# Optimization experiments

Measured on AMD Instinct MI355X. Metric: run time of the kernel, lower is better.

## Reference

```python
import jax, jax.numpy as jnp
import numpy as np

N = 8192
NT = 85       # number of DFIRE atom types
BINS = 28     # distance bins, d/0.7 clamped to [0,27]
EXCLU = 2     # nbre_nt_exclu


def setup_inputs() -> dict:
    key = jax.random.key(0)
    k1, k2, k3, k4 = jax.random.split(key, 4)
    # coords scaled so pairwise distances span the 0..19.6A cutoff range
    coords = jax.random.normal(k1, (N, 3), dtype=jnp.float32) * 10.0
    res_ids = jnp.sort(jax.random.randint(k2, (N,), 0, 400)).astype(jnp.int32)
    type_indices = jax.random.randint(k3, (N,), 0, NT).astype(jnp.int32)
    pot = jax.random.normal(k4, (NT, NT, BINS), dtype=jnp.float32)
    # original LUT is symmetric in the two type axes
    pot_tensor = 0.5 * (pot + jnp.transpose(pot, (1, 0, 2)))
    # upper-triangular pair indices, offset=1 (deterministic, like torch.triu_indices)
    ii, jj = np.triu_indices(N, 1)
    i_idx = jnp.asarray(ii, dtype=jnp.int32)
    j_idx = jnp.asarray(jj, dtype=jnp.int32)
    return {
        "coords": coords,
        "pot_tensor": pot_tensor,
        "res_ids": res_ids,
        "type_indices": type_indices,
        "i_idx": i_idx,
        "j_idx": j_idx,
    }


def reference(coords, pot_tensor, res_ids, type_indices, i_idx, j_idx):
    # sequence-separation and valid-type mask (stream compaction -> masked sum)
    sep = jnp.abs(res_ids[i_idx] - res_ids[j_idx])
    t1 = type_indices[i_idx]
    t2 = type_indices[j_idx]
    mask = (sep > EXCLU) & (t1 >= 0) & (t2 >= 0)

    # pairwise distances on all triu pairs
    diff = coords[i_idx] - coords[j_idx]              # [P,3]
    dists = jnp.sqrt(jnp.sum(diff * diff, axis=1)) + 1e-8  # [P]

    # bin + linear interpolation from the 3D LUT
    d_scaled = dists / 0.7
    d0 = jnp.floor(jnp.clip(d_scaled, 0.0, 27.0)).astype(jnp.int32)
    d1 = jnp.minimum(d0 + 1, 27)
    alpha = d_scaled - d0.astype(dists.dtype)

    # safe indices for masked-out pairs (their energy is multiplied by 0)
    t1s = jnp.where(mask, t1, 0)
    t2s = jnp.where(mask, t2, 0)
    e0 = pot_tensor[t1s, t2s, d0]
    e1 = pot_tensor[t1s, t2s, d1]
    energy = (1.0 - alpha) * e0 + alpha * e1

    w = mask & (dists < 19.6)
    return jnp.sum(energy * w.astype(energy.dtype))
```

## Files before the change

kernel.cpp:

```cpp
#include <hip/hip_runtime.h>

#define NT    85
#define BINS  28
#define LUT_ELEMS (NT * NT * BINS)
#define CUT2  (19.6f * 19.6f)
#define ROWCAP 8
#define COLCAP 8

__device__ __forceinline__ unsigned bf16r(float x) {
    unsigned b = __float_as_uint(x);
    return (b + 0x7FFFu + ((b >> 16) & 1u)) >> 16;
}

__global__ __launch_bounds__(256) void prep_k(const float* __restrict__ pot,
                                              const int* __restrict__ type, int N,
                                              unsigned* __restrict__ pk,
                                              int* __restrict__ offs) {
    if ((int)blockIdx.x == (int)gridDim.x - 1) {
        __shared__ int h[NT];
        for (int t = threadIdx.x; t < NT; t += 256) h[t] = 0;
        __syncthreads();
        for (int i = threadIdx.x; i < N; i += 256) atomicAdd(&h[type[i]], 1);
        __syncthreads();
        if (threadIdx.x == 0) {
            int s = 0;
            for (int t = 0; t < NT; ++t) { int c = h[t]; offs[t] = s; s += c; }
        }
    }
    int idx = blockIdx.x * 256 + threadIdx.x;
    if (idx < LUT_ELEMS) {
        int d  = idx % BINS;
        int ab = idx / BINS;
        int d1 = (d + 1 < BINS) ? d + 1 : BINS - 1;
        float e0 = pot[idx], e1 = pot[ab * BINS + d1];
        pk[idx] = (bf16r(e1) << 16) | bf16r(e0);
    }
}

__global__ void scatter_k(const float* __restrict__ coords, const int* __restrict__ res,
                          const int* __restrict__ type, int* __restrict__ offs,
                          float4* __restrict__ pc, int N) {
    int i = blockIdx.x * blockDim.x + threadIdx.x;
    if (i >= N) return;
    int t = type[i];
    int p = atomicAdd(&offs[t], 1);
    pc[p] = make_float4(coords[3 * i], coords[3 * i + 1], coords[3 * i + 2],
                        __int_as_float((t << 10) | res[i]));
}

__global__ __launch_bounds__(128) void dfire_pairs6(
    const float4*  __restrict__ pc,
    const unsigned* __restrict__ pk,
    float* __restrict__ partial, int TI, int TJ) {

    __shared__ float4   jtile[128];
    __shared__ unsigned lrow[ROWCAP * COLCAP * BINS];
    __shared__ float    wsum[2];

    int k = blockIdx.x;
    double A = (double)TJ + 1.0;
    int ri = (int)((A - sqrt(A * A - 4.0 * (double)k)) * 0.5);
    if (ri < 0) ri = 0;
    if (ri > TI - 1) ri = TI - 1;
    while (ri > 0 && ri * (TJ + 1 - ri) > k) --ri;
    while (ri + 1 < TI && (ri + 1) * (TJ + 1 - (ri + 1)) <= k) ++ri;
    int cj = 2 * ri + (k - ri * (TJ + 1 - ri));

    int bi = ri * 256, bj = cj * 128;
    int tid = threadIdx.x;

    jtile[tid] = pc[bj + tid];

    float4 ci0 = pc[bi + tid];
    float4 ci1 = pc[bi + 128 + tid];

    const int* pci = (const int*)pc;
    int tA = pci[4 * bi + 3] >> 10;
    int tB = pci[4 * (bi + 255) + 3] >> 10;
    int tC = pci[4 * bj + 3] >> 10;
    int tD = pci[4 * (bj + 127) + 3] >> 10;
    int nrow = tB - tA + 1, ncol = tD - tC + 1;
    bool useLds = (nrow <= ROWCAP) && (ncol <= COLCAP);

    if (useLds) {
        int tot = nrow * ncol * BINS;
        for (int e = tid; e < tot; e += 128) {
            int d  = e % BINS;
            int rc = e / BINS;
            int cc = rc % ncol;
            int rr = rc / ncol;
            lrow[e] = pk[((tA + rr) * NT + (tC + cc)) * BINS + d];
        }
    }
    __syncthreads();

    int w0 = __float_as_int(ci0.w), w1 = __float_as_int(ci1.w);
    int ires0 = w0 & 1023, ires1 = w1 & 1023;
    int it0 = w0 >> 10, it1 = w1 >> 10;
    int rb0 = (it0 - tA) * (ncol * BINS);
    int rb1 = (it1 - tA) * (ncol * BINS);
    int gb0 = it0 * (NT * BINS);
    int gb1 = it1 * (NT * BINS);
    bool straddle = (cj <= 2 * ri + 1);
    int ig0 = straddle ? (bi + tid)       : -1;
    int ig1 = straddle ? (bi + 128 + tid) : -1;

    float acc0 = 0.f, acc1 = 0.f;
    int w = tid >> 6;

#define PAIR(CI, IRES, IG, RBASE, ACC) do {                                   \
    float dx = (CI).x - cj4.x, dy = (CI).y - cj4.y, dz = (CI).z - cj4.z;      \
    float d2 = fmaf(dx, dx, fmaf(dy, dy, dz * dz));                           \
    int sep = (IRES) - jres; sep = sep < 0 ? -sep : sep;                      \
    bool v = (sep > 2) & (d2 < CUT2) & (jg > (IG));                           \
    float dist  = __builtin_amdgcn_sqrtf(d2);                                 \
    float ds    = dist * (1.0f / 0.7f);                                       \
    float dsc   = fminf(ds, 27.0f);                                           \
    int   d0    = (int)dsc;                                                   \
    float alpha = ds - (float)d0;                                             \
    unsigned u  = SRC[(RBASE) + jcb + d0];                                    \
    float e0 = __uint_as_float(u << 16);                                      \
    float e1 = __uint_as_float(u & 0xFFFF0000u);                              \
    float en = fmaf(alpha, e1 - e0, e0);                                      \
    ACC += v ? en : 0.0f;                                                     \
} while (0)

    if (useLds) {
        #pragma unroll 4
        for (int s = 0; s < 128; ++s) {
            int j = (s + (w << 6)) & 127;
            float4 cj4 = jtile[j];
            int wj  = __builtin_amdgcn_readfirstlane(__float_as_int(cj4.w));
            int jres = wj & 1023;
            int jcb  = ((wj >> 10) - tC) * BINS;
            int jg   = bj + j;
#define SRC lrow
            PAIR(ci0, ires0, ig0, rb0, acc0);
            PAIR(ci1, ires1, ig1, rb1, acc1);
#undef SRC
        }
    } else {
        #pragma unroll 2
        for (int s = 0; s < 128; ++s) {
            int j = (s + (w << 6)) & 127;
            float4 cj4 = jtile[j];
            int wj  = __builtin_amdgcn_readfirstlane(__float_as_int(cj4.w));
            int jres = wj & 1023;
            int jcb  = (wj >> 10) * BINS;
            int jg   = bj + j;
#define SRC pk
            PAIR(ci0, ires0, ig0, gb0, acc0);
            PAIR(ci1, ires1, ig1, gb1, acc1);
#undef SRC
        }
    }
#undef PAIR

    float acc = acc0 + acc1;
    for (int off = 32; off > 0; off >>= 1)
        acc += __shfl_down(acc, off, 64);
    if ((tid & 63) == 0) wsum[tid >> 6] = acc;
    __syncthreads();
    if (tid == 0) partial[blockIdx.x] = wsum[0] + wsum[1];
}

__global__ __launch_bounds__(256) void reduce_k(const float* __restrict__ p, int n,
                                                float* __restrict__ out) {
    __shared__ float ws[4];
    float a = 0.f;
    for (int i = threadIdx.x; i < n; i += 256) a += p[i];
    for (int off = 32; off > 0; off >>= 1)
        a += __shfl_down(a, off, 64);
    if ((threadIdx.x & 63) == 0) ws[threadIdx.x >> 6] = a;
    __syncthreads();
    if (threadIdx.x == 0) out[0] = (ws[0] + ws[1]) + (ws[2] + ws[3]);
}

__global__ __launch_bounds__(256) void dfire_pairs_fb(
    const float* __restrict__ coords, const int* __restrict__ res,
    const int* __restrict__ type, const float* __restrict__ pot,
    float* __restrict__ out, int T) {

    __shared__ float jx[128], jy[128], jz[128];
    __shared__ int   jres[128], jtype[128];

    int k = blockIdx.x;
    int r = (int)((2.0 * T + 1.0 - sqrt((2.0 * T + 1.0) * (2.0 * T + 1.0) - 8.0 * (double)k)) * 0.5);
    if (r < 0) r = 0;
    if (r > T - 1) r = T - 1;
    while (r > 0 && (r * T - r * (r - 1) / 2) > k) --r;
    while (((r + 1) * T - (r + 1) * r / 2) <= k) ++r;
    int c = r + (k - (r * T - r * (r - 1) / 2));

    int bi = r * 128, bj = c * 128;
    int tid = threadIdx.x;
    if (tid < 128) {
        int gj = bj + tid;
        jx[tid] = coords[3 * gj]; jy[tid] = coords[3 * gj + 1]; jz[tid] = coords[3 * gj + 2];
        jres[tid] = res[gj]; jtype[tid] = type[gj];
    }
    int ii = tid & 127;
    int gi = bi + ii;
    float ix = coords[3 * gi], iy = coords[3 * gi + 1], iz = coords[3 * gi + 2];
    int iresv = res[gi], it = type[gi];
    int ii_eff = (bi == bj) ? ii : -1;
    __syncthreads();

    float acc = 0.f;
    int jj = tid >> 7;
    for (int s = 0; s < 64; ++s, jj += 2) {
        float dx = ix - jx[jj], dy = iy - jy[jj], dz = iz - jz[jj];
        float d2 = dx * dx + dy * dy + dz * dz;
        float dist = sqrtf(d2) + 1e-8f;
        int sep = abs(iresv - jres[jj]);
        bool v = (sep > 2) & (dist < 19.6f) & (jj > ii_eff);
        if (v) {
            float ds = dist * (1.0f / 0.7f);
            int d0 = (int)fminf(ds, 27.0f);
            int d1 = (d0 + 1 < BINS) ? d0 + 1 : BINS - 1;
            float alpha = ds - (float)d0;
            int row = (jtype[jj] * NT + it) * BINS;
            float e0 = pot[row + d0], e1 = pot[row + d1];
            acc += e0 + alpha * (e1 - e0);
        }
    }
    for (int off = 32; off > 0; off >>= 1)
        acc += __shfl_down(acc, off, 64);
    if ((tid & 63) == 0) atomicAdd(out, acc);
}

extern "C" void kernel_launch(void* const* d_in, const int* in_sizes, int n_in,
                              void* d_out, int out_size, void* d_ws, size_t ws_size,
                              hipStream_t stream) {
    const float* coords = (const float*)d_in[0];
    const float* pot    = (const float*)d_in[1];
    const int*   res    = (const int*)d_in[2];
    const int*   type   = (const int*)d_in[3];

    const int N = in_sizes[2];
    float* out = (float*)d_out;

    const int TI = N / 256, TJ = N / 128;
    const int nblk = TI * (TJ + 1 - TI);

    const size_t pkBytes   = (size_t)LUT_ELEMS * sizeof(unsigned);
    const size_t pcBytes   = (size_t)N * sizeof(float4);
    const size_t offsBytes = 128 * sizeof(int);
    const size_t partBytes = (size_t)nblk * sizeof(float);
    const size_t need = pkBytes + pcBytes + offsBytes + partBytes;

    if (ws_size >= need && (N % 256) == 0) {
        char* w = (char*)d_ws;
        unsigned* pk      = (unsigned*)w;   w += pkBytes;
        float4*   pc      = (float4*)w;     w += pcBytes;
        int*      offs    = (int*)w;        w += offsBytes;
        float*    partial = (float*)w;

        const int prepBlocks = (LUT_ELEMS + 255) / 256;
        prep_k<<<prepBlocks + 1, 256, 0, stream>>>(pot, type, N, pk, offs);
        scatter_k<<<(N + 255) / 256, 256, 0, stream>>>(coords, res, type, offs, pc, N);
        dfire_pairs6<<<nblk, 128, 0, stream>>>(pc, pk, partial, TI, TJ);
        reduce_k<<<1, 256, 0, stream>>>(partial, nblk, out);
    } else {
        hipMemsetAsync(out, 0, sizeof(float), stream);
        const int T = N / 128;
        dfire_pairs_fb<<<T * (T + 1) / 2, 256, 0, stream>>>(coords, res, type, pot, out, T);
    }
}
```

Before: 286.8 us.

## Fuse prep, scatter, pair and reduce kernels into one cooperative kernel

Replaces the four-kernel pipeline with a single cooperative launch that packs the LUT, sorts atoms by type in one block, computes pair energies, and reduces partials, separated by grid-wide syncs. The pair tiling changes to 512-row by 64-column tiles with 256-thread blocks. The aim is to remove launch gaps and intermediate kernel boundaries. In exchange, the scatter is serialized into one block and grid syncs add barrier cost, with the old path kept as a fallback.

```diff
diff --git a/kernel.cpp b/kernel.cpp
--- a/kernel.cpp
+++ b/kernel.cpp
@@ -1,7 +1,11 @@
 #include <hip/hip_runtime.h>
+#include <hip/hip_cooperative_groups.h>
+
+namespace cg = cooperative_groups;
 
 #define NT    85
 #define BINS  28
+#define NTB   (NT * BINS)
 #define LUT_ELEMS (NT * NT * BINS)
 #define CUT2  (19.6f * 19.6f)
 #define ROWCAP 8
@@ -12,101 +16,97 @@
     return (b + 0x7FFFu + ((b >> 16) & 1u)) >> 16;
 }
 
-__global__ __launch_bounds__(256) void prep_k(const float* __restrict__ pot,
-                                              const int* __restrict__ type, int N,
-                                              unsigned* __restrict__ pk,
-                                              int* __restrict__ offs) {
-    if ((int)blockIdx.x == (int)gridDim.x - 1) {
-        __shared__ int h[NT];
-        for (int t = threadIdx.x; t < NT; t += 256) h[t] = 0;
-        __syncthreads();
-        for (int i = threadIdx.x; i < N; i += 256) atomicAdd(&h[type[i]], 1);
-        __syncthreads();
-        if (threadIdx.x == 0) {
-            int s = 0;
-            for (int t = 0; t < NT; ++t) { int c = h[t]; offs[t] = s; s += c; }
-        }
-    }
-    int idx = blockIdx.x * 256 + threadIdx.x;
+__global__ __launch_bounds__(256) void fused_k(
+    const float* __restrict__ pot, const float* __restrict__ coords,
+    const int* __restrict__ res, const int* __restrict__ type,
+    unsigned* __restrict__ pk, float4* __restrict__ pc,
+    float* __restrict__ partial, float* __restrict__ out,
+    int N, int TI, int TJ) {
+
+    cg::grid_group grid = cg::this_grid();
+
+    __shared__ float4   jtile[64];
+    __shared__ unsigned lrow[ROWCAP * COLCAP * BINS];
+    __shared__ float    wsum[4];
+
+    const int tid = threadIdx.x;
+    const int bid = blockIdx.x;
+    const int nb  = (int)gridDim.x;
+
+    int idx = bid * 256 + tid;
     if (idx < LUT_ELEMS) {
         int d  = idx % BINS;
         int ab = idx / BINS;
         int d1 = (d + 1 < BINS) ? d + 1 : BINS - 1;
-        float e0 = pot[idx], e1 = pot[ab * BINS + d1];
-        pk[idx] = (bf16r(e1) << 16) | bf16r(e0);
-    }
-}
-
-__global__ void scatter_k(const float* __restrict__ coords, const int* __restrict__ res,
-                          const int* __restrict__ type, int* __restrict__ offs,
-                          float4* __restrict__ pc, int N) {
-    int i = blockIdx.x * blockDim.x + threadIdx.x;
-    if (i >= N) return;
-    int t = type[i];
-    int p = atomicAdd(&offs[t], 1);
-    pc[p] = make_float4(coords[3 * i], coords[3 * i + 1], coords[3 * i + 2],
-                        __int_as_float((t << 10) | res[i]));
-}
-
-__global__ __launch_bounds__(128) void dfire_pairs6(
-    const float4*  __restrict__ pc,
-    const unsigned* __restrict__ pk,
-    float* __restrict__ partial, int TI, int TJ) {
-
-    __shared__ float4   jtile[128];
-    __shared__ unsigned lrow[ROWCAP * COLCAP * BINS];
-    __shared__ float    wsum[2];
-
-    int k = blockIdx.x;
-    double A = (double)TJ + 1.0;
-    int ri = (int)((A - sqrt(A * A - 4.0 * (double)k)) * 0.5);
-    if (ri < 0) ri = 0;
-    if (ri > TI - 1) ri = TI - 1;
-    while (ri > 0 && ri * (TJ + 1 - ri) > k) --ri;
-    while (ri + 1 < TI && (ri + 1) * (TJ + 1 - (ri + 1)) <= k) ++ri;
-    int cj = 2 * ri + (k - ri * (TJ + 1 - ri));
-
-    int bi = ri * 256, bj = cj * 128;
-    int tid = threadIdx.x;
-
-    jtile[tid] = pc[bj + tid];
-
-    float4 ci0 = pc[bi + tid];
-    float4 ci1 = pc[bi + 128 + tid];
-
-    const int* pci = (const int*)pc;
-    int tA = pci[4 * bi + 3] >> 10;
-    int tB = pci[4 * (bi + 255) + 3] >> 10;
-    int tC = pci[4 * bj + 3] >> 10;
-    int tD = pci[4 * (bj + 127) + 3] >> 10;
-    int nrow = tB - tA + 1, ncol = tD - tC + 1;
-    bool useLds = (nrow <= ROWCAP) && (ncol <= COLCAP);
-
-    if (useLds) {
-        int tot = nrow * ncol * BINS;
-        for (int e = tid; e < tot; e += 128) {
-            int d  = e % BINS;
-            int rc = e / BINS;
-            int cc = rc % ncol;
-            int rr = rc / ncol;
-            lrow[e] = pk[((tA + rr) * NT + (tC + cc)) * BINS + d];
-        }
-    }
-    __syncthreads();
-
-    int w0 = __float_as_int(ci0.w), w1 = __float_as_int(ci1.w);
-    int ires0 = w0 & 1023, ires1 = w1 & 1023;
-    int it0 = w0 >> 10, it1 = w1 >> 10;
-    int rb0 = (it0 - tA) * (ncol * BINS);
-    int rb1 = (it1 - tA) * (ncol * BINS);
-    int gb0 = it0 * (NT * BINS);
-    int gb1 = it1 * (NT * BINS);
-    bool straddle = (cj <= 2 * ri + 1);
-    int ig0 = straddle ? (bi + tid)       : -1;
-    int ig1 = straddle ? (bi + 128 + tid) : -1;
-
-    float acc0 = 0.f, acc1 = 0.f;
-    int w = tid >> 6;
+        pk[idx] = (bf16r(pot[ab * BINS + d1]) << 16) | bf16r(pot[idx]);
+    }
+    if (bid == nb - 1) {
+        int* h  = (int*)lrow;
+        int* of = h + 128;
+        if (tid < NT) h[tid] = 0;
+        __syncthreads();
+        for (int i = tid; i < N; i += 256) atomicAdd(&h[type[i]], 1);
+        __syncthreads();
+        if (tid == 0) { int s = 0; for (int t = 0; t < NT; ++t) { of[t] = s; s += h[t]; } }
+        __syncthreads();
+        for (int i = tid; i < N; i += 256) {
+            int t = type[i];
+            int p = atomicAdd(&of[t], 1);
+            pc[p] = make_float4(coords[3 * i], coords[3 * i + 1], coords[3 * i + 2],
+                                __int_as_float((t << 10) | res[i]));
+        }
+    }
+    grid.sync();
+
+    {
+        int k = bid;
+        double A = (double)TJ + 4.0;
+        int ri = (int)((A - sqrt(A * A - 16.0 * (double)k)) / 8.0);
+        if (ri < 0) ri = 0;
+        if (ri > TI - 1) ri = TI - 1;
+        while (ri > 0 && ri * (TJ + 4 - 4 * ri) > k) --ri;
+        while (ri + 1 < TI && (ri + 1) * (TJ + 4 - 4 * (ri + 1)) <= k) ++ri;
+        int cj = 8 * ri + (k - ri * (TJ + 4 - 4 * ri));
+
+        int bi = ri * 512, bj = cj * 64;
+
+        if (tid < 64) jtile[tid] = pc[bj + tid];
+        float4 ci0 = pc[bi + tid];
+        float4 ci1 = pc[bi + 256 + tid];
+
+        const int* pci = (const int*)pc;
+        int tA = pci[4 * bi + 3] >> 10;
+        int tB = pci[4 * (bi + 511) + 3] >> 10;
+        int tC = pci[4 * bj + 3] >> 10;
+        int tD = pci[4 * (bj + 63) + 3] >> 10;
+        int nrow = tB - tA + 1, ncol = tD - tC + 1;
+        bool useLds = (nrow <= ROWCAP) && (ncol <= COLCAP);
+
+        if (useLds) {
+            int tot = nrow * ncol * BINS;
+            for (int e = tid; e < tot; e += 256) {
+                int d  = e % BINS;
+                int rc = e / BINS;
+                int cc = rc % ncol;
+                int rr = rc / ncol;
+                lrow[e] = pk[((tA + rr) * NT + (tC + cc)) * BINS + d];
+            }
+        }
+        __syncthreads();
+
+        int w0 = __float_as_int(ci0.w), w1 = __float_as_int(ci1.w);
+        int ires0 = w0 & 1023, ires1 = w1 & 1023;
+        int it0 = w0 >> 10, it1 = w1 >> 10;
+        int rb0 = (it0 - tA) * (ncol * BINS);
+        int rb1 = (it1 - tA) * (ncol * BINS);
+        int gb0 = it0 * NTB;
+        int gb1 = it1 * NTB;
+        bool straddle = (cj < 8 * ri + 8);
+        int ig0 = straddle ? (bi + tid)       : -1;
+        int ig1 = straddle ? (bi + 256 + tid) : -1;
+
+        float acc0 = 0.f, acc1 = 0.f;
+        int woff = (tid >> 6) << 4;
 
 #define PAIR(CI, IRES, IG, RBASE, ACC) do {                                   \
     float dx = (CI).x - cj4.x, dy = (CI).y - cj4.y, dz = (CI).z - cj4.z;      \
@@ -125,6 +125,168 @@
     ACC += v ? en : 0.0f;                                                     \
 } while (0)
 
+        if (useLds) {
+            #pragma unroll 4
+            for (int s = 0; s < 64; ++s) {
+                int j = (s + woff) & 63;
+                float4 cj4 = jtile[j];
+                int wj   = __builtin_amdgcn_readfirstlane(__float_as_int(cj4.w));
+                int jres = wj & 1023;
+                int jcb  = ((wj >> 10) - tC) * BINS;
+                int jg   = bj + j;
+#define SRC lrow
+                PAIR(ci0, ires0, ig0, rb0, acc0);
+                PAIR(ci1, ires1, ig1, rb1, acc1);
+#undef SRC
+            }
+        } else {
+            #pragma unroll 2
+            for (int s = 0; s < 64; ++s) {
+                int j = (s + woff) & 63;
+                float4 cj4 = jtile[j];
+                int wj   = __builtin_amdgcn_readfirstlane(__float_as_int(cj4.w));
+                int jres = wj & 1023;
+                int jcb  = (wj >> 10) * BINS;
+#define SRC pk
+                int jg   = bj + j;
+                PAIR(ci0, ires0, ig0, gb0, acc0);
+                PAIR(ci1, ires1, ig1, gb1, acc1);
+#undef SRC
+            }
+        }
+#undef PAIR
+
+        float acc = acc0 + acc1;
+        for (int off = 32; off > 0; off >>= 1)
+            acc += __shfl_down(acc, off, 64);
+        if ((tid & 63) == 0) wsum[tid >> 6] = acc;
+        __syncthreads();
+        if (tid == 0) partial[bid] = (wsum[0] + wsum[1]) + (wsum[2] + wsum[3]);
+    }
+    grid.sync();
+
+    if (bid == 0) {
+        float a = 0.f;
+        for (int i = tid; i < nb; i += 256) a += partial[i];
+        for (int off = 32; off > 0; off >>= 1)
+            a += __shfl_down(a, off, 64);
+        if ((tid & 63) == 0) wsum[tid >> 6] = a;
+        __syncthreads();
+        if (tid == 0) out[0] = (wsum[0] + wsum[1]) + (wsum[2] + wsum[3]);
+    }
+}
+
+__global__ __launch_bounds__(256) void prep_k(const float* __restrict__ pot,
+                                              const int* __restrict__ type, int N,
+                                              unsigned* __restrict__ pk,
+                                              int* __restrict__ offs) {
+    if ((int)blockIdx.x == (int)gridDim.x - 1) {
+        __shared__ int h[NT];
+        for (int t = threadIdx.x; t < NT; t += 256) h[t] = 0;
+        __syncthreads();
+        for (int i = threadIdx.x; i < N; i += 256) atomicAdd(&h[type[i]], 1);
+        __syncthreads();
+        if (threadIdx.x == 0) {
+            int s = 0;
+            for (int t = 0; t < NT; ++t) { offs[t] = s; s += h[t]; }
+        }
+    }
+    int idx = blockIdx.x * 256 + threadIdx.x;
+    if (idx < LUT_ELEMS) {
+        int d  = idx % BINS;
+        int ab = idx / BINS;
+        int d1 = (d + 1 < BINS) ? d + 1 : BINS - 1;
+        pk[idx] = (bf16r(pot[ab * BINS + d1]) << 16) | bf16r(pot[idx]);
+    }
+}
+
+__global__ void scatter_k(const float* __restrict__ coords, const int* __restrict__ res,
+                          const int* __restrict__ type, int* __restrict__ offs,
+                          float4* __restrict__ pc, int N) {
+    int i = blockIdx.x * blockDim.x + threadIdx.x;
+    if (i >= N) return;
+    int t = type[i];
+    int p = atomicAdd(&offs[t], 1);
+    pc[p] = make_float4(coords[3 * i], coords[3 * i + 1], coords[3 * i + 2],
+                        __int_as_float((t << 10) | res[i]));
+}
+
+__global__ __launch_bounds__(128) void dfire_pairs6(
+    const float4*  __restrict__ pc,
+    const unsigned* __restrict__ pk,
+    float* __restrict__ partial, int TI, int TJ) {
+
+    __shared__ float4   jtile[128];
+    __shared__ unsigned lrow[ROWCAP * COLCAP * BINS];
+    __shared__ float    wsum[2];
+
+    int k = blockIdx.x;
+    double A = (double)TJ + 1.0;
+    int ri = (int)((A - sqrt(A * A - 4.0 * (double)k)) * 0.5);
+    if (ri < 0) ri = 0;
+    if (ri > TI - 1) ri = TI - 1;
+    while (ri > 0 && ri * (TJ + 1 - ri) > k) --ri;
+    while (ri + 1 < TI && (ri + 1) * (TJ + 1 - (ri + 1)) <= k) ++ri;
+    int cj = 2 * ri + (k - ri * (TJ + 1 - ri));
+
+    int bi = ri * 256, bj = cj * 128;
+    int tid = threadIdx.x;
+
+    jtile[tid] = pc[bj + tid];
+    float4 ci0 = pc[bi + tid];
+    float4 ci1 = pc[bi + 128 + tid];
+
+    const int* pci = (const int*)pc;
+    int tA = pci[4 * bi + 3] >> 10;
+    int tB = pci[4 * (bi + 255) + 3] >> 10;
+    int tC = pci[4 * bj + 3] >> 10;
+    int tD = pci[4 * (bj + 127) + 3] >> 10;
+    int nrow = tB - tA + 1, ncol = tD - tC + 1;
+    bool useLds = (nrow <= ROWCAP) && (ncol <= COLCAP);
+
+    if (useLds) {
+        int tot = nrow * ncol * BINS;
+        for (int e = tid; e < tot; e += 128) {
+            int d  = e % BINS;
+            int rc = e / BINS;
+            int cc = rc % ncol;
+            int rr = rc / ncol;
+            lrow[e] = pk[((tA + rr) * NT + (tC + cc)) * BINS + d];
+        }
+    }
+    __syncthreads();
+
+    int w0 = __float_as_int(ci0.w), w1 = __float_as_int(ci1.w);
+    int ires0 = w0 & 1023, ires1 = w1 & 1023;
+    int it0 = w0 >> 10, it1 = w1 >> 10;
+    int rb0 = (it0 - tA) * (ncol * BINS);
+    int rb1 = (it1 - tA) * (ncol * BINS);
+    int gb0 = it0 * NTB;
+    int gb1 = it1 * NTB;
+    bool straddle = (cj <= 2 * ri + 1);
+    int ig0 = straddle ? (bi + tid)       : -1;
+    int ig1 = straddle ? (bi + 128 + tid) : -1;
+
+    float acc0 = 0.f, acc1 = 0.f;
+    int w = tid >> 6;
+
+#define PAIR(CI, IRES, IG, RBASE, ACC) do {                                   \
+    float dx = (CI).x - cj4.x, dy = (CI).y - cj4.y, dz = (CI).z - cj4.z;      \
+    float d2 = fmaf(dx, dx, fmaf(dy, dy, dz * dz));                           \
+    int sep = (IRES) - jres; sep = sep < 0 ? -sep : sep;                      \
+    bool v = (sep > 2) & (d2 < CUT2) & (jg > (IG));                           \
+    float dist  = __builtin_amdgcn_sqrtf(d2);                                 \
+    float ds    = dist * (1.0f / 0.7f);                                       \
+    float dsc   = fminf(ds, 27.0f);                                           \
+    int   d0    = (int)dsc;                                                   \
+    float alpha = ds - (float)d0;                                             \
+    unsigned u  = SRC[(RBASE) + jcb + d0];                                    \
+    float e0 = __uint_as_float(u << 16);                                      \
+    float e1 = __uint_as_float(u & 0xFFFF0000u);                              \
+    float en = fmaf(alpha, e1 - e0, e0);                                      \
+    ACC += v ? en : 0.0f;                                                     \
+} while (0)
+
     if (useLds) {
         #pragma unroll 4
         for (int s = 0; s < 128; ++s) {
@@ -240,27 +402,45 @@
     const int N = in_sizes[2];
     float* out = (float*)d_out;
 
-    const int TI = N / 256, TJ = N / 128;
-    const int nblk = TI * (TJ + 1 - TI);
-
-    const size_t pkBytes   = (size_t)LUT_ELEMS * sizeof(unsigned);
+    const size_t pkBytes   = (((size_t)(LUT_ELEMS + 1) * 4) + 15) & ~(size_t)15;
     const size_t pcBytes   = (size_t)N * sizeof(float4);
     const size_t offsBytes = 128 * sizeof(int);
-    const size_t partBytes = (size_t)nblk * sizeof(float);
+    const size_t partBytes = 4096 * sizeof(float);
     const size_t need = pkBytes + pcBytes + offsBytes + partBytes;
 
-    if (ws_size >= need && (N % 256) == 0) {
+    if (ws_size >= need && (N % 512) == 0) {
         char* w = (char*)d_ws;
         unsigned* pk      = (unsigned*)w;   w += pkBytes;
         float4*   pc      = (float4*)w;     w += pcBytes;
         int*      offs    = (int*)w;        w += offsBytes;
         float*    partial = (float*)w;
 
+        int coop = 0, dev = 0;
+        hipGetDevice(&dev);
+        hipDeviceGetAttribute(&coop, hipDeviceAttributeCooperativeLaunch, dev);
+
+        if (coop) {
+            int TI = N / 512, TJ = N / 64;
+            int nblk = TI * (TJ + 4 - 4 * TI);
+            const float* a_pot = pot; const float* a_co = coords;
+            const int* a_res = res; const int* a_ty = type;
+            unsigned* a_pk = pk; float4* a_pc = pc; float* a_pa = partial;
+            float* a_out = out; int a_N = N, a_TI = TI, a_TJ = TJ;
+            void* args[] = { &a_pot, &a_co, &a_res, &a_ty, &a_pk, &a_pc,
+                             &a_pa, &a_out, &a_N, &a_TI, &a_TJ };
+            hipError_t e = hipLaunchCooperativeKernel((const void*)fused_k,
+                                dim3(nblk), dim3(256), args, 0, stream);
+            if (e == hipSuccess) return;
+            (void)hipGetLastError();
+        }
+
+        int TI2 = N / 256, TJ2 = N / 128;
+        int nblk2 = TI2 * (TJ2 + 1 - TI2);
         const int prepBlocks = (LUT_ELEMS + 255) / 256;
         prep_k<<<prepBlocks + 1, 256, 0, stream>>>(pot, type, N, pk, offs);
         scatter_k<<<(N + 255) / 256, 256, 0, stream>>>(coords, res, type, offs, pc, N);
-        dfire_pairs6<<<nblk, 128, 0, stream>>>(pc, pk, partial, TI, TJ);
-        reduce_k<<<1, 256, 0, stream>>>(partial, nblk, out);
+        dfire_pairs6<<<nblk2, 128, 0, stream>>>(pc, pk, partial, TI2, TJ2);
+        reduce_k<<<1, 256, 0, stream>>>(partial, nblk2, out);
     } else {
         hipMemsetAsync(out, 0, sizeof(float), stream);
         const int T = N / 128;
```

Result: slower. 501.2 us (+74.8%).

## Switch pair kernel to 128x128 triangular tiles split across 256 threads

Applied to the files above, without the earlier changes.

The pair kernel now uses square 128x128 tiles over the upper triangle instead of 256x128 tiles. Each block has 256 threads, and each thread handles one i atom over half of the j tile, where the old layout had one thread per two i atoms over all of j. The j loop is fully unrolled with four independent accumulators, and launch bounds request higher occupancy. This aims to give smaller type ranges per tile, so the LDS LUT path is taken more often, and more parallelism and ILP per block. The cost is twice as many blocks, more reductions, and more redundant tile loads.

```diff
diff --git a/kernel.cpp b/kernel.cpp
--- a/kernel.cpp
+++ b/kernel.cpp
@@ -2,6 +2,7 @@
 
 #define NT    85
 #define BINS  28
+#define NTB   (NT * BINS)
 #define LUT_ELEMS (NT * NT * BINS)
 #define CUT2  (19.6f * 19.6f)
 #define ROWCAP 8
@@ -24,16 +25,16 @@
         __syncthreads();
         if (threadIdx.x == 0) {
             int s = 0;
-            for (int t = 0; t < NT; ++t) { int c = h[t]; offs[t] = s; s += c; }
-        }
+            for (int t = 0; t < NT; ++t) { offs[t] = s; s += h[t]; }
+        }
+        return;
     }
     int idx = blockIdx.x * 256 + threadIdx.x;
     if (idx < LUT_ELEMS) {
         int d  = idx % BINS;
         int ab = idx / BINS;
         int d1 = (d + 1 < BINS) ? d + 1 : BINS - 1;
-        float e0 = pot[idx], e1 = pot[ab * BINS + d1];
-        pk[idx] = (bf16r(e1) << 16) | bf16r(e0);
+        pk[idx] = (bf16r(pot[ab * BINS + d1]) << 16) | bf16r(pot[idx]);
     }
 }
 
@@ -48,35 +49,34 @@
                         __int_as_float((t << 10) | res[i]));
 }
 
-__global__ __launch_bounds__(128) void dfire_pairs6(
+__global__ __launch_bounds__(256, 8) void dfire_pairs8(
     const float4*  __restrict__ pc,
     const unsigned* __restrict__ pk,
-    float* __restrict__ partial, int TI, int TJ) {
+    float* __restrict__ partial, int T) {
 
     __shared__ float4   jtile[128];
     __shared__ unsigned lrow[ROWCAP * COLCAP * BINS];
-    __shared__ float    wsum[2];
+    __shared__ float    wsum[4];
 
     int k = blockIdx.x;
-    double A = (double)TJ + 1.0;
-    int ri = (int)((A - sqrt(A * A - 4.0 * (double)k)) * 0.5);
-    if (ri < 0) ri = 0;
-    if (ri > TI - 1) ri = TI - 1;
-    while (ri > 0 && ri * (TJ + 1 - ri) > k) --ri;
-    while (ri + 1 < TI && (ri + 1) * (TJ + 1 - (ri + 1)) <= k) ++ri;
-    int cj = 2 * ri + (k - ri * (TJ + 1 - ri));
-
-    int bi = ri * 256, bj = cj * 128;
+    int r = (int)((2.0 * T + 1.0 - sqrt((2.0 * T + 1.0) * (2.0 * T + 1.0) - 8.0 * (double)k)) * 0.5);
+    if (r < 0) r = 0;
+    if (r > T - 1) r = T - 1;
+    while (r > 0 && (r * T - r * (r - 1) / 2) > k) --r;
+    while (((r + 1) * T - (r + 1) * r / 2) <= k) ++r;
+    int c = r + (k - (r * T - r * (r - 1) / 2));
+
+    int bi = r * 128, bj = c * 128;
     int tid = threadIdx.x;
 
-    jtile[tid] = pc[bj + tid];
-
-    float4 ci0 = pc[bi + tid];
-    float4 ci1 = pc[bi + 128 + tid];
+    if (tid < 128) jtile[tid] = pc[bj + tid];
+
+    int ii = tid & 127;
+    float4 ci = pc[bi + ii];
 
     const int* pci = (const int*)pc;
     int tA = pci[4 * bi + 3] >> 10;
-    int tB = pci[4 * (bi + 255) + 3] >> 10;
+    int tB = pci[4 * (bi + 127) + 3] >> 10;
     int tC = pci[4 * bj + 3] >> 10;
     int tD = pci[4 * (bj + 127) + 3] >> 10;
     int nrow = tB - tA + 1, ncol = tD - tC + 1;
@@ -84,7 +84,7 @@
 
     if (useLds) {
         int tot = nrow * ncol * BINS;
-        for (int e = tid; e < tot; e += 128) {
+        for (int e = tid; e < tot; e += 256) {
             int d  = e % BINS;
             int rc = e / BINS;
             int cc = rc % ncol;
@@ -94,25 +94,25 @@
     }
     __syncthreads();
 
-    int w0 = __float_as_int(ci0.w), w1 = __float_as_int(ci1.w);
-    int ires0 = w0 & 1023, ires1 = w1 & 1023;
-    int it0 = w0 >> 10, it1 = w1 >> 10;
-    int rb0 = (it0 - tA) * (ncol * BINS);
-    int rb1 = (it1 - tA) * (ncol * BINS);
-    int gb0 = it0 * (NT * BINS);
-    int gb1 = it1 * (NT * BINS);
-    bool straddle = (cj <= 2 * ri + 1);
-    int ig0 = straddle ? (bi + tid)       : -1;
-    int ig1 = straddle ? (bi + 128 + tid) : -1;
-
-    float acc0 = 0.f, acc1 = 0.f;
-    int w = tid >> 6;
-
-#define PAIR(CI, IRES, IG, RBASE, ACC) do {                                   \
-    float dx = (CI).x - cj4.x, dy = (CI).y - cj4.y, dz = (CI).z - cj4.z;      \
+    int wi   = __float_as_int(ci.w);
+    int ires = wi & 1023;
+    int it   = wi >> 10;
+    int rbL  = (it - tA) * (ncol * BINS);
+    int rbG  = it * NTB;
+    int ii_eff = (bi == bj) ? ii : -1;
+
+    float a0 = 0.f, a1 = 0.f, a2 = 0.f, a3 = 0.f;
+    int w = tid >> 7;
+
+#define PAIR(J, RBASE, ACC) do {                                              \
+    float4 cj4 = jtile[(J)];                                                  \
+    int  wj   = __builtin_amdgcn_readfirstlane(__float_as_int(cj4.w));        \
+    int  jres = wj & 1023;                                                    \
+    int  jcb  = CBASE(wj);                                                    \
+    float dx = ci.x - cj4.x, dy = ci.y - cj4.y, dz = ci.z - cj4.z;            \
     float d2 = fmaf(dx, dx, fmaf(dy, dy, dz * dz));                           \
-    int sep = (IRES) - jres; sep = sep < 0 ? -sep : sep;                      \
-    bool v = (sep > 2) & (d2 < CUT2) & (jg > (IG));                           \
+    int sep = ires - jres; sep = sep < 0 ? -sep : sep;                        \
+    bool v = (sep > 2) & (d2 < CUT2) & ((J) > ii_eff);                        \
     float dist  = __builtin_amdgcn_sqrtf(d2);                                 \
     float ds    = dist * (1.0f / 0.7f);                                       \
     float dsc   = fminf(ds, 27.0f);                                           \
@@ -126,42 +126,40 @@
 } while (0)
 
     if (useLds) {
-        #pragma unroll 4
-        for (int s = 0; s < 128; ++s) {
-            int j = (s + (w << 6)) & 127;
-            float4 cj4 = jtile[j];
-            int wj  = __builtin_amdgcn_readfirstlane(__float_as_int(cj4.w));
-            int jres = wj & 1023;
-            int jcb  = ((wj >> 10) - tC) * BINS;
-            int jg   = bj + j;
 #define SRC lrow
-            PAIR(ci0, ires0, ig0, rb0, acc0);
-            PAIR(ci1, ires1, ig1, rb1, acc1);
+#define CBASE(WJ) ((((WJ) >> 10) - tC) * BINS)
+        #pragma unroll
+        for (int s = 0; s < 16; ++s) {
+            int j = 8 * s + w;
+            PAIR(j,     rbL, a0);
+            PAIR(j + 2, rbL, a1);
+            PAIR(j + 4, rbL, a2);
+            PAIR(j + 6, rbL, a3);
+        }
+#undef CBASE
 #undef SRC
-        }
     } else {
-        #pragma unroll 2
-        for (int s = 0; s < 128; ++s) {
-            int j = (s + (w << 6)) & 127;
-            float4 cj4 = jtile[j];
-            int wj  = __builtin_amdgcn_readfirstlane(__float_as_int(cj4.w));
-            int jres = wj & 1023;
-            int jcb  = (wj >> 10) * BINS;
-            int jg   = bj + j;
 #define SRC pk
-            PAIR(ci0, ires0, ig0, gb0, acc0);
-            PAIR(ci1, ires1, ig1, gb1, acc1);
+#define CBASE(WJ) (((WJ) >> 10) * BINS)
+        #pragma unroll
+        for (int s = 0; s < 16; ++s) {
+            int j = 8 * s + w;
+            PAIR(j,     rbG, a0);
+            PAIR(j + 2, rbG, a1);
+            PAIR(j + 4, rbG, a2);
+            PAIR(j + 6, rbG, a3);
+        }
+#undef CBASE
 #undef SRC
-        }
     }
 #undef PAIR
 
-    float acc = acc0 + acc1;
+    float acc = (a0 + a1) + (a2 + a3);
     for (int off = 32; off > 0; off >>= 1)
         acc += __shfl_down(acc, off, 64);
     if ((tid & 63) == 0) wsum[tid >> 6] = acc;
     __syncthreads();
-    if (tid == 0) partial[blockIdx.x] = wsum[0] + wsum[1];
+    if (tid == 0) partial[blockIdx.x] = (wsum[0] + wsum[1]) + (wsum[2] + wsum[3]);
 }
 
 __global__ __launch_bounds__(256) void reduce_k(const float* __restrict__ p, int n,
@@ -240,16 +238,16 @@
     const int N = in_sizes[2];
     float* out = (float*)d_out;
 
-    const int TI = N / 256, TJ = N / 128;
-    const int nblk = TI * (TJ + 1 - TI);
-
-    const size_t pkBytes   = (size_t)LUT_ELEMS * sizeof(unsigned);
+    const int T = N / 128;
+    const int nblk = T * (T + 1) / 2;
+
+    const size_t pkBytes   = (((size_t)LUT_ELEMS * 4) + 15) & ~(size_t)15;
     const size_t pcBytes   = (size_t)N * sizeof(float4);
     const size_t offsBytes = 128 * sizeof(int);
     const size_t partBytes = (size_t)nblk * sizeof(float);
     const size_t need = pkBytes + pcBytes + offsBytes + partBytes;
 
-    if (ws_size >= need && (N % 256) == 0) {
+    if (ws_size >= need && (N % 128) == 0) {
         char* w = (char*)d_ws;
         unsigned* pk      = (unsigned*)w;   w += pkBytes;
         float4*   pc      = (float4*)w;     w += pcBytes;
@@ -259,11 +257,10 @@
         const int prepBlocks = (LUT_ELEMS + 255) / 256;
         prep_k<<<prepBlocks + 1, 256, 0, stream>>>(pot, type, N, pk, offs);
         scatter_k<<<(N + 255) / 256, 256, 0, stream>>>(coords, res, type, offs, pc, N);
-        dfire_pairs6<<<nblk, 128, 0, stream>>>(pc, pk, partial, TI, TJ);
+        dfire_pairs8<<<nblk, 256, 0, stream>>>(pc, pk, partial, T);
         reduce_k<<<1, 256, 0, stream>>>(partial, nblk, out);
     } else {
         hipMemsetAsync(out, 0, sizeof(float), stream);
-        const int T = N / 128;
         dfire_pairs_fb<<<T * (T + 1) / 2, 256, 0, stream>>>(coords, res, type, pot, out, T);
     }
 }
```

New measurement: 322.3 us. 1.12x slower.
